# Kernel optimization log

Measured on AMD Instinct MI355X. Metric: run time of the kernel, lower is better.

The kernel has to match this reference:

```python
import jax, jax.numpy as jnp
import numpy as np

N = 50000      # nodes
E = 600000     # edges
C = 32         # in_features (channels)
COUT = 32      # out_features
NB = 8         # n_basis
NS = 10        # n_species
H = 64         # radial MLP hidden
NPATH = 5      # uvu paths for l_max=1: (0,0,0),(0,1,1),(1,0,1),(1,1,0),(1,1,1)
AVG = 12.0     # avg_n_neighbors
RS = 1.6765324703310907  # rescaled SiLU constant


def _rescaled_silu(x):
    return RS * jax.nn.silu(x)


def setup_inputs() -> dict:
    key = jax.random.key(0)
    ks = jax.random.split(key, 16)
    return {
        'node_attrs': jax.random.uniform(ks[0], (N, NS), dtype=jnp.float32),
        'node_feats': jax.random.normal(ks[1], (N, C, 4), dtype=jnp.float32),
        'edge_attrs': jax.random.normal(ks[2], (E, 1, 4), dtype=jnp.float32),
        'edge_feats': jax.random.normal(ks[3], (E, NB), dtype=jnp.float32),
        'W_first': jax.random.normal(ks[4], (2, C, C), dtype=jnp.float32),
        'Wr0': jax.random.normal(ks[5], (H, NB), dtype=jnp.float32),
        'Wr1': jax.random.normal(ks[6], (H, H), dtype=jnp.float32),
        'Wr2': jax.random.normal(ks[7], (H, H), dtype=jnp.float32),
        'Wr3': jax.random.normal(ks[8], (NPATH * C, H), dtype=jnp.float32),
        'W_second0': jax.random.normal(ks[9], (COUT, 2 * C), dtype=jnp.float32),
        'W_second1': jax.random.normal(ks[10], (COUT, 3 * C), dtype=jnp.float32),
        'W_skip': jax.random.normal(ks[11], (2, C, NS, C), dtype=jnp.float32),
        'idx_i': jnp.sort(jax.random.randint(ks[12], (E,), 0, N)),
        'idx_j': jax.random.randint(ks[13], (E,), 0, N),
    }


def reference(node_attrs, node_feats, edge_attrs, edge_feats, W_first, Wr0, Wr1,
              Wr2, Wr3, W_second0, W_second1, W_skip, idx_i, idx_j):
    # ---- skip_tp: uvw tensor product with l=0 node_attrs (species-dependent mixing per l)
    sc0 = jnp.einsum('ncm,nv,cvw->nwm', node_feats[:, :, :1], node_attrs, W_skip[0]) / np.sqrt(C * NS)
    sc1 = jnp.einsum('ncm,nv,cvw->nwm', node_feats[:, :, 1:4], node_attrs, W_skip[1]) / np.sqrt(C * NS)
    sc = jnp.concatenate([sc0, sc1], axis=-1)  # [N, C, 4]

    # ---- linear_first: per-l channel mixing
    x0 = jnp.einsum('ncm,dc->ndm', node_feats[:, :, :1], W_first[0]) / np.sqrt(C)   # [N,C,1]
    x1 = jnp.einsum('ncm,dc->ndm', node_feats[:, :, 1:4], W_first[1]) / np.sqrt(C)  # [N,C,3]

    # ---- radial MLP: Linear+RescaledSiLU chain, last SiLU dropped
    h = _rescaled_silu(edge_feats @ Wr0.T / np.sqrt(NB))
    h = _rescaled_silu(h @ Wr1.T / np.sqrt(H))
    h = _rescaled_silu(h @ Wr2.T / np.sqrt(H))
    w = (h @ Wr3.T / np.sqrt(H)).reshape(E, NPATH, C)  # per-edge, per-path, per-channel weights

    # ---- gather sender features
    xj0 = x0[idx_j][:, :, 0]   # [E, C]
    xj1 = x1[idx_j]            # [E, C, 3]
    y0 = edge_attrs[:, 0, 0]   # [E]      l=0 harmonic
    y1 = edge_attrs[:, 0, 1:4] # [E, 3]   l=1 harmonic

    # ---- uvu weighted tensor product (l_max=1 CG: scalar mult, dot, cross)
    p0 = w[:, 0] * xj0 * y0[:, None]                                   # (0,0,0) -> l=0
    p1 = w[:, 1, :, None] * xj0[:, :, None] * y1[:, None, :]          # (0,1,1) -> l=1
    p2 = w[:, 2, :, None] * xj1 * y0[:, None, None]                   # (1,0,1) -> l=1
    p3 = w[:, 3] * jnp.einsum('ecm,em->ec', xj1, y1)                  # (1,1,0) -> l=0
    p4 = w[:, 4, :, None] * jnp.cross(xj1, y1[:, None, :])            # (1,1,1) -> l=1

    # ---- scatter-add messages to receivers
    seg = lambda m: jax.ops.segment_sum(m, idx_i, num_segments=N)
    msg0 = seg(jnp.stack([p0, p3], axis=1))  # [N, 2, C]
    msg1 = seg(jnp.stack([p1, p2, p4], axis=1))  # [N, 3, C, 3]

    # ---- linear_second: mix (paths x channels) -> out_features per l
    out0 = jnp.einsum('npc,dpc->nd', msg0, W_second0.reshape(COUT, 2, C)) / np.sqrt(2 * C)
    out1 = jnp.einsum('npcm,dpc->ndm', msg1, W_second1.reshape(COUT, 3, C)) / np.sqrt(3 * C)
    message = jnp.concatenate([out0[:, :, None], out1], axis=-1) / AVG  # [N, COUT, 4]
    return message, sc
```

## Files before the change

kernel.cpp:

```cpp
#include <hip/hip_runtime.h>
#include <math.h>

#define N_NODES 50000
#define N_EDGES 600000

constexpr float RS          = 1.6765324703310907f;
constexpr float INV_SQRT8   = 0.35355339059327373f;
constexpr float INV8        = 0.125f;
constexpr float INV_SQRT320 = 0.05590169943749474f;
constexpr float INV_SQRT32  = 0.17677669529663687f;
constexpr float INV_SQRT96  = 0.10206207261596575f;
constexpr float INV_AVG     = 1.0f / 12.0f;

constexpr size_t OFF_X     = 0;
constexpr size_t OFF_ROW   = 25600000;
constexpr size_t OFF_FRAG  = 25800064;
constexpr size_t OFF_FRAG2 = 25841024;
constexpr size_t OFF_W     = 25931136;

typedef __attribute__((ext_vector_type(8))) short bfrag;
typedef __attribute__((ext_vector_type(4))) float ffrag;

__device__ __forceinline__ float rsilu(float z) {
  float t = __builtin_amdgcn_exp2f(z * -1.44269504088896341f);
  return (RS * z) * __builtin_amdgcn_rcpf(1.0f + t);
}
__device__ __forceinline__ unsigned short f2bf(float x) {
  unsigned u = __float_as_uint(x);
  u += 0x7FFFu + ((u >> 16) & 1u);
  return (unsigned short)(u >> 16);
}
__device__ __forceinline__ float bf2f(unsigned short u) {
  return __uint_as_float(((unsigned)u) << 16);
}

__global__ __launch_bounds__(256) void k_rowstart(const int* __restrict__ idx_i,
                                                  int* __restrict__ row,
                                                  int E, int N) {
  int e = blockIdx.x * 256 + threadIdx.x;
  if (e >= E) return;
  int cur  = idx_i[e];
  int prev = (e == 0) ? -1 : idx_i[e - 1];
  for (int n = prev + 1; n <= cur; ++n) row[n] = e;
  if (e == E - 1) {
    for (int n = cur + 1; n <= N; ++n) row[n] = E;
  }
}

__global__ __launch_bounds__(256) void k_prep(const float* __restrict__ Wr0,
                                              const float* __restrict__ Wr1,
                                              const float* __restrict__ Wr2,
                                              const float* __restrict__ Wr3,
                                              unsigned short* __restrict__ frag) {
  int t = blockIdx.x * 256 + threadIdx.x;
  int f    = t >> 9;
  int lane = (t >> 3) & 63;
  int j    = t & 7;
  int n16  = lane & 15, quad = lane >> 4;
  float v;
  if (f < 4) {
    int d = f * 16 + n16, k = quad * 8 + j;
    v = (k < 8) ? Wr0[d * 8 + k] * INV_SQRT8 : 0.f;
  } else if (f < 12) {
    int ff = f - 4, ntile = ff >> 1, ks = ff & 1;
    int d = ntile * 16 + n16, k = ks * 32 + quad * 8 + j;
    v = Wr1[d * 64 + k] * INV8;
  } else if (f < 20) {
    int ff = f - 12, ntile = ff >> 1, ks = ff & 1;
    int d = ntile * 16 + n16, k = ks * 32 + quad * 8 + j;
    v = Wr2[d * 64 + k] * INV8;
  } else {
    int ff = f - 20, ntile = ff >> 1, ks = ff & 1;
    int d = ntile * 16 + n16, k = ks * 32 + quad * 8 + j;
    v = Wr3[d * 64 + k] * INV8;
  }
  frag[t] = f2bf(v);
}

__global__ __launch_bounds__(256) void k_prep2(const float* __restrict__ Wsk,
                                               const float* __restrict__ Wf,
                                               unsigned short* __restrict__ frag2) {
  int t = blockIdx.x * 256 + threadIdx.x;
  int f    = t >> 9;
  int lane = (t >> 3) & 63;
  int j    = t & 7;
  int n16  = lane & 15, quad = lane >> 4;
  int ks = f >> 3, nt = f & 7;
  int k   = ks * 32 + quad * 8 + j;
  int col = nt * 16 + n16;
  float v = 0.f;
  if (k < 320) {
    int vv = k >> 5, c = k & 31;
    if (col < 32)       v = Wsk[(c * 10 + vv) * 32 + col] * INV_SQRT320;
    else if (col < 64)  v = Wsk[((32 + c) * 10 + vv) * 32 + (col - 32)] * INV_SQRT320;
  } else {
    int c = k - 320;
    if (col >= 96)      v = Wf[1024 + (col - 96) * 32 + c] * INV_SQRT32;
    else if (col >= 64) v = Wf[(col - 64) * 32 + c] * INV_SQRT32;
  }
  frag2[t] = f2bf(v);
}

__global__ __launch_bounds__(256) void k_node_mfma(const float* __restrict__ attrs,
                                                   const float* __restrict__ feats,
                                                   const unsigned short* __restrict__ frag2,
                                                   float* __restrict__ out_sc,
                                                   float* __restrict__ x_ws) {
  int tid = threadIdx.x;
  int wave = tid >> 6, lane = tid & 63;
  int quad = lane >> 4, l16 = lane & 15;
  int nb = blockIdx.x * 32 + wave * 8;

  float featsF[2][8];
  float a[2][10];
#pragma unroll
  for (int mt = 0; mt < 2; ++mt) {
    int nodeA = nb + mt * 4 + (l16 >> 2);
    if (nodeA > N_NODES - 1) nodeA = N_NODES - 1;
    int m = l16 & 3;
#pragma unroll
    for (int j = 0; j < 8; ++j)
      featsF[mt][j] = feats[(size_t)nodeA * 128 + (quad * 8 + j) * 4 + m];
#pragma unroll
    for (int v = 0; v < 10; ++v) a[mt][v] = attrs[nodeA * 10 + v];
  }

  ffrag acc[2][8];
#pragma unroll
  for (int mt = 0; mt < 2; ++mt)
#pragma unroll
    for (int nt = 0; nt < 8; ++nt) acc[mt][nt] = (ffrag){0.f, 0.f, 0.f, 0.f};

#pragma unroll
  for (int ks = 0; ks < 11; ++ks) {
    bfrag Ab[2];
#pragma unroll
    for (int mt = 0; mt < 2; ++mt) {
      union { unsigned short s8[8]; bfrag v; } pk;
#pragma unroll
      for (int j = 0; j < 8; ++j) {
        float val = (ks < 10) ? a[mt][ks] * featsF[mt][j] : featsF[mt][j];
        pk.s8[j] = f2bf(val);
      }
      Ab[mt] = pk.v;
    }
#pragma unroll
    for (int nt = 0; nt < 8; ++nt) {
      bfrag B = *(const bfrag*)(frag2 + ((size_t)(ks * 8 + nt) * 64 + lane) * 8);
      acc[0][nt] = __builtin_amdgcn_mfma_f32_16x16x32_bf16(Ab[0], B, acc[0][nt], 0, 0, 0);
      acc[1][nt] = __builtin_amdgcn_mfma_f32_16x16x32_bf16(Ab[1], B, acc[1][nt], 0, 0, 0);
    }
  }

#pragma unroll
  for (int mt = 0; mt < 2; ++mt) {
    int node = nb + mt * 4 + quad;
    if (node < N_NODES) {
      float4 sc0 = {acc[mt][0][0], acc[mt][2][1], acc[mt][2][2], acc[mt][2][3]};
      float4 sc1 = {acc[mt][1][0], acc[mt][3][1], acc[mt][3][2], acc[mt][3][3]};
      float4 x0  = {acc[mt][4][0], acc[mt][6][1], acc[mt][6][2], acc[mt][6][3]};
      float4 x1  = {acc[mt][5][0], acc[mt][7][1], acc[mt][7][2], acc[mt][7][3]};
      ((float4*)out_sc)[(size_t)node * 32 + l16]      = sc0;
      ((float4*)out_sc)[(size_t)node * 32 + 16 + l16] = sc1;
      ((float4*)x_ws)[(size_t)node * 32 + l16]        = x0;
      ((float4*)x_ws)[(size_t)node * 32 + 16 + l16]   = x1;
    }
  }
}

#define MLP_M 128
__global__ __launch_bounds__(256) void k_mlp(const float* __restrict__ ef,
                                             const unsigned short* __restrict__ frag,
                                             unsigned short* __restrict__ w_out,
                                             int E) {
  __shared__ __align__(16) unsigned short H[4][32][168];
  int tid = threadIdx.x;
  int wave = tid >> 6, lane = tid & 63;
  int quad = lane >> 4, l16 = lane & 15;
  int m0 = blockIdx.x * MLP_M + wave * 32;
  unsigned short (*Hw)[168] = H[wave];

  bfrag a1[2];
#pragma unroll
  for (int mt = 0; mt < 2; ++mt) {
    float vals[8] = {0.f, 0.f, 0.f, 0.f, 0.f, 0.f, 0.f, 0.f};
    if (quad == 0) {
      int r = m0 + mt * 16 + l16;
      if (r > E - 1) r = E - 1;
      const float4* p = (const float4*)(ef + (size_t)r * 8);
      float4 u0 = p[0], u1 = p[1];
      vals[0] = u0.x; vals[1] = u0.y; vals[2] = u0.z; vals[3] = u0.w;
      vals[4] = u1.x; vals[5] = u1.y; vals[6] = u1.z; vals[7] = u1.w;
    }
    union { unsigned short s[8]; bfrag v; } pk;
#pragma unroll
    for (int j = 0; j < 8; ++j) pk.s[j] = f2bf(vals[j]);
    a1[mt] = pk.v;
  }
#pragma unroll
  for (int nt = 0; nt < 4; ++nt) {
    const bfrag* bp = (const bfrag*)(frag + ((size_t)(nt) * 64 + lane) * 8);
    bfrag b = *bp;
    ffrag acc0 = {0.f, 0.f, 0.f, 0.f}, acc1 = acc0;
    acc0 = __builtin_amdgcn_mfma_f32_16x16x32_bf16(a1[0], b, acc0, 0, 0, 0);
    acc1 = __builtin_amdgcn_mfma_f32_16x16x32_bf16(a1[1], b, acc1, 0, 0, 0);
#pragma unroll
    for (int r = 0; r < 4; ++r) {
      Hw[0 * 16 + quad * 4 + r][nt * 16 + l16] = f2bf(rsilu(acc0[r]));
      Hw[1 * 16 + quad * 4 + r][nt * 16 + l16] = f2bf(rsilu(acc1[r]));
    }
  }

  bfrag A[2][2];
#pragma unroll 1
  for (int L = 0; L < 2; ++L) {
    int fbase = 4 + L * 8;
#pragma unroll
    for (int mt = 0; mt < 2; ++mt)
#pragma unroll
      for (int ks = 0; ks < 2; ++ks)
        A[mt][ks] = *(const bfrag*)&Hw[mt * 16 + l16][ks * 32 + quad * 8];
#pragma unroll
    for (int nt = 0; nt < 4; ++nt) {
      ffrag acc0 = {0.f, 0.f, 0.f, 0.f}, acc1 = acc0;
#pragma unroll
      for (int ks = 0; ks < 2; ++ks) {
        bfrag b = *(const bfrag*)(frag + ((size_t)(fbase + nt * 2 + ks) * 64 + lane) * 8);
        acc0 = __builtin_amdgcn_mfma_f32_16x16x32_bf16(A[0][ks], b, acc0, 0, 0, 0);
        acc1 = __builtin_amdgcn_mfma_f32_16x16x32_bf16(A[1][ks], b, acc1, 0, 0, 0);
      }
#pragma unroll
      for (int r = 0; r < 4; ++r) {
        Hw[0 * 16 + quad * 4 + r][nt * 16 + l16] = f2bf(rsilu(acc0[r]));
        Hw[1 * 16 + quad * 4 + r][nt * 16 + l16] = f2bf(rsilu(acc1[r]));
      }
    }
  }

#pragma unroll
  for (int mt = 0; mt < 2; ++mt)
#pragma unroll
    for (int ks = 0; ks < 2; ++ks)
      A[mt][ks] = *(const bfrag*)&Hw[mt * 16 + l16][ks * 32 + quad * 8];
#pragma unroll 2
  for (int nt = 0; nt < 10; ++nt) {
    ffrag acc0 = {0.f, 0.f, 0.f, 0.f}, acc1 = acc0;
#pragma unroll
    for (int ks = 0; ks < 2; ++ks) {
      bfrag b = *(const bfrag*)(frag + ((size_t)(20 + nt * 2 + ks) * 64 + lane) * 8);
      acc0 = __builtin_amdgcn_mfma_f32_16x16x32_bf16(A[0][ks], b, acc0, 0, 0, 0);
      acc1 = __builtin_amdgcn_mfma_f32_16x16x32_bf16(A[1][ks], b, acc1, 0, 0, 0);
    }
    int col = nt * 16 + l16;
    int p = col >> 5, cc = col & 31;
    int ncol = (p < 4) ? ((p >> 1) * 64 + 2 * cc + (p & 1)) : (128 + cc);
#pragma unroll
    for (int r = 0; r < 4; ++r) {
      Hw[0 * 16 + quad * 4 + r][ncol] = f2bf(acc0[r]);
      Hw[1 * 16 + quad * 4 + r][ncol] = f2bf(acc1[r]);
    }
  }

  {
    int row = lane / 20, off = lane - row * 20;
    int grow_base = m0;
#pragma unroll 2
    for (int it = 0; it < 10; ++it) {
      int grow = grow_base + row;
      uint4 v = *(const uint4*)&Hw[row][off * 8];
      if (grow < E)
        *(uint4*)(w_out + (size_t)grow * 160 + off * 8) = v;
      off += 4;
      row += 3;
      if (off >= 20) { off -= 20; row += 1; }
    }
  }
}

__global__ __launch_bounds__(256) void k_msg(const unsigned short* __restrict__ w_ws,
                                             const float* __restrict__ x_ws,
                                             const float* __restrict__ ea,
                                             const int* __restrict__ idx_j,
                                             const int* __restrict__ row,
                                             const float* __restrict__ Ws0,
                                             const float* __restrict__ Ws1,
                                             float* __restrict__ out_msg) {
  __shared__ __align__(16) float msg[8][356];

  int tid = threadIdx.x;
  int ln = tid >> 5, c = tid & 31;
  int n = blockIdx.x * 8 + ln;
  int e0 = row[n], e1 = row[n + 1];

  float m00 = 0.f, m01 = 0.f;
  float m10x = 0.f, m10y = 0.f, m10z = 0.f;
  float m11x = 0.f, m11y = 0.f, m11z = 0.f;
  float m12x = 0.f, m12y = 0.f, m12z = 0.f;

  for (int base = e0; base < e1; base += 32) {
    int rem = e1 - base;
    int cnt = rem < 32 ? rem : 32;
    int jidx = base + (c < cnt ? c : cnt - 1);
    int j_c = __builtin_nontemporal_load(idx_j + jidx);

    for (int b = 0; b < cnt; b += 4) {
      int mvalid = cnt - b;
      float4 xj[4], y4[4];
      unsigned d01[4], d23[4];
      unsigned short w4v[4];
#pragma unroll
      for (int t = 0; t < 4; ++t) {
        int tt = (t < mvalid) ? t : 0;
        int e = base + b + tt;
        int j = __shfl(j_c, b + tt, 32);
        xj[t] = ((const float4*)x_ws)[(size_t)j * 32 + c];
        y4[t] = ((const float4*)ea)[e];
        const char* wb = (const char*)w_ws + (size_t)e * 320;
        d01[t] = *(const unsigned*)(wb + 4 * c);
        d23[t] = *(const unsigned*)(wb + 128 + 4 * c);
        w4v[t] = *(const unsigned short*)(wb + 256 + 2 * c);
      }
#pragma unroll
      for (int t = 0; t < 4; ++t) {
        if (t < mvalid) {
          float w0 = __uint_as_float(d01[t] << 16);
          float w1 = __uint_as_float(d01[t] & 0xffff0000u);
          float w2 = __uint_as_float(d23[t] << 16);
          float w3 = __uint_as_float(d23[t] & 0xffff0000u);
          float w4 = bf2f(w4v[t]);
          float4 x4 = xj[t], yy = y4[t];
          m00 += w0 * x4.x * yy.x;
          m01 += w3 * (x4.y * yy.y + x4.z * yy.z + x4.w * yy.w);
          m10x += w1 * x4.x * yy.y;
          m10y += w1 * x4.x * yy.z;
          m10z += w1 * x4.x * yy.w;
          m11x += w2 * x4.y * yy.x;
          m11y += w2 * x4.z * yy.x;
          m11z += w2 * x4.w * yy.x;
          float cx = x4.z * yy.w - x4.w * yy.z;
          float cy = x4.w * yy.y - x4.y * yy.w;
          float cz = x4.y * yy.z - x4.z * yy.y;
          m12x += w4 * cx;
          m12y += w4 * cy;
          m12z += w4 * cz;
        }
      }
    }
  }

  msg[ln][c]      = m00;
  msg[ln][32 + c] = m01;
  msg[ln][64 + 0 * 96 +  0 + c] = m10x;
  msg[ln][64 + 0 * 96 + 32 + c] = m11x;
  msg[ln][64 + 0 * 96 + 64 + c] = m12x;
  msg[ln][64 + 1 * 96 +  0 + c] = m10y;
  msg[ln][64 + 1 * 96 + 32 + c] = m11y;
  msg[ln][64 + 1 * 96 + 64 + c] = m12y;
  msg[ln][64 + 2 * 96 +  0 + c] = m10z;
  msg[ln][64 + 2 * 96 + 32 + c] = m11z;
  msg[ln][64 + 2 * 96 + 64 + c] = m12z;
  __syncthreads();

  int wv = tid >> 6;
  int lane = tid & 63;
  int quad = lane >> 4, l16 = lane & 15;
  int nb = blockIdx.x * 8;

  const float* WS   = (wv == 0) ? Ws0 : Ws1;
  int   K      = (wv == 0) ? 64 : 96;
  int   mbase  = (wv == 0) ? 0 : 64 + (wv - 1) * 96;
  float oscale = (wv == 0) ? (INV8 * INV_AVG) : (INV_SQRT96 * INV_AVG);

  ffrag acc0 = {0.f, 0.f, 0.f, 0.f}, acc1 = acc0;
  const float* arow = &msg[l16 & 7][mbase + quad * 8];
#pragma unroll 1
  for (int ks = 0; ks < K; ks += 32) {
    float4 a0 = *(const float4*)(arow + ks);
    float4 a1 = *(const float4*)(arow + ks + 4);
    union { unsigned short s[8]; bfrag v; } pa;
    pa.s[0] = f2bf(a0.x); pa.s[1] = f2bf(a0.y); pa.s[2] = f2bf(a0.z); pa.s[3] = f2bf(a0.w);
    pa.s[4] = f2bf(a1.x); pa.s[5] = f2bf(a1.y); pa.s[6] = f2bf(a1.z); pa.s[7] = f2bf(a1.w);

    const float* bp0 = WS + (size_t)l16 * K + ks + quad * 8;
    const float* bp1 = bp0 + (size_t)16 * K;
    {
      float4 b0 = *(const float4*)(bp0);
      float4 b1 = *(const float4*)(bp0 + 4);
      union { unsigned short s[8]; bfrag v; } pb;
      pb.s[0] = f2bf(b0.x * oscale); pb.s[1] = f2bf(b0.y * oscale);
      pb.s[2] = f2bf(b0.z * oscale); pb.s[3] = f2bf(b0.w * oscale);
      pb.s[4] = f2bf(b1.x * oscale); pb.s[5] = f2bf(b1.y * oscale);
      pb.s[6] = f2bf(b1.z * oscale); pb.s[7] = f2bf(b1.w * oscale);
      acc0 = __builtin_amdgcn_mfma_f32_16x16x32_bf16(pa.v, pb.v, acc0, 0, 0, 0);
    }
    {
      float4 b0 = *(const float4*)(bp1);
      float4 b1 = *(const float4*)(bp1 + 4);
      union { unsigned short s[8]; bfrag v; } pb;
      pb.s[0] = f2bf(b0.x * oscale); pb.s[1] = f2bf(b0.y * oscale);
      pb.s[2] = f2bf(b0.z * oscale); pb.s[3] = f2bf(b0.w * oscale);
      pb.s[4] = f2bf(b1.x * oscale); pb.s[5] = f2bf(b1.y * oscale);
      pb.s[6] = f2bf(b1.z * oscale); pb.s[7] = f2bf(b1.w * oscale);
      acc1 = __builtin_amdgcn_mfma_f32_16x16x32_bf16(pa.v, pb.v, acc1, 0, 0, 0);
    }
  }

#pragma unroll
  for (int r = 0; r < 4; ++r) {
    int rowv = quad * 4 + r;
    if (rowv < 8) {
      size_t base = (size_t)(nb + rowv) * 128 + (size_t)l16 * 4 + wv;
      out_msg[base]      = acc0[r];
      out_msg[base + 64] = acc1[r];
    }
  }
}

extern "C" void kernel_launch(void* const* d_in, const int* in_sizes, int n_in,
                              void* d_out, int out_size, void* d_ws, size_t ws_size,
                              hipStream_t stream) {
  const float* node_attrs = (const float*)d_in[0];
  const float* node_feats = (const float*)d_in[1];
  const float* edge_attrs = (const float*)d_in[2];
  const float* edge_feats = (const float*)d_in[3];
  const float* W_first    = (const float*)d_in[4];
  const float* Wr0        = (const float*)d_in[5];
  const float* Wr1        = (const float*)d_in[6];
  const float* Wr2        = (const float*)d_in[7];
  const float* Wr3        = (const float*)d_in[8];
  const float* Ws0        = (const float*)d_in[9];
  const float* Ws1        = (const float*)d_in[10];
  const float* Wsk        = (const float*)d_in[11];
  const int*   idx_i      = (const int*)d_in[12];
  const int*   idx_j      = (const int*)d_in[13];
  float* out = (float*)d_out;

  char* ws = (char*)d_ws;
  float*          x_ws   = (float*)(ws + OFF_X);
  int*            rowp   = (int*)(ws + OFF_ROW);
  unsigned short* fragp  = (unsigned short*)(ws + OFF_FRAG);
  unsigned short* frag2p = (unsigned short*)(ws + OFF_FRAG2);
  unsigned short* w_ws   = (unsigned short*)(ws + OFF_W);

  k_rowstart<<<(N_EDGES + 255) / 256, 256, 0, stream>>>(idx_i, rowp, N_EDGES, N_NODES);
  k_prep<<<80, 256, 0, stream>>>(Wr0, Wr1, Wr2, Wr3, fragp);
  k_prep2<<<176, 256, 0, stream>>>(Wsk, W_first, frag2p);
  k_node_mfma<<<(N_NODES + 31) / 32, 256, 0, stream>>>(node_attrs, node_feats,
                                                       frag2p, out + 6400000, x_ws);
  k_mlp<<<(N_EDGES + MLP_M - 1) / MLP_M, 256, 0, stream>>>(edge_feats, fragp,
                                                           w_ws, N_EDGES);
  k_msg<<<N_NODES / 8, 256, 0, stream>>>(w_ws, x_ws, edge_attrs, idx_j, rowp,
                                         Ws0, Ws1, out);
}
```

Before: 333.7 us.

## Assign one full wavefront per node in k_msg, splitting edges across half-waves

The message kernel now gives each node a 64-lane wavefront instead of a 32-lane half-wave. The two halves process alternating groups of 4 edges and combine their partial sums with a cross-half shuffle before writing to shared memory. Block size doubles to 512, and only the first 4 waves run the output MFMA stage. This is meant to shorten the per-node serial edge loop and expose more memory-level parallelism for the gathers, at the cost of more threads per node, idle waves in the epilogue, and extra reduction shuffles.

```diff
diff --git a/kernel.cpp b/kernel.cpp
--- a/kernel.cpp
+++ b/kernel.cpp
@@ -277,7 +277,7 @@
   }
 }
 
-__global__ __launch_bounds__(256) void k_msg(const unsigned short* __restrict__ w_ws,
+__global__ __launch_bounds__(512) void k_msg(const unsigned short* __restrict__ w_ws,
                                              const float* __restrict__ x_ws,
                                              const float* __restrict__ ea,
                                              const int* __restrict__ idx_j,
@@ -288,8 +288,11 @@
   __shared__ __align__(16) float msg[8][356];
 
   int tid = threadIdx.x;
-  int ln = tid >> 5, c = tid & 31;
-  int n = blockIdx.x * 8 + ln;
+  int wv = tid >> 6;
+  int lane = tid & 63;
+  int c = lane & 31;
+  int h = lane >> 5;
+  int n = blockIdx.x * 8 + wv;
   int e0 = row[n], e1 = row[n + 1];
 
   float m00 = 0.f, m01 = 0.f;
@@ -297,22 +300,23 @@
   float m11x = 0.f, m11y = 0.f, m11z = 0.f;
   float m12x = 0.f, m12y = 0.f, m12z = 0.f;
 
-  for (int base = e0; base < e1; base += 32) {
+  for (int base = e0; base < e1; base += 64) {
     int rem = e1 - base;
-    int cnt = rem < 32 ? rem : 32;
-    int jidx = base + (c < cnt ? c : cnt - 1);
+    int cnt = rem < 64 ? rem : 64;
+    int jidx = base + (lane < cnt ? lane : cnt - 1);
     int j_c = __builtin_nontemporal_load(idx_j + jidx);
 
-    for (int b = 0; b < cnt; b += 4) {
-      int mvalid = cnt - b;
+    for (int bb = 0; bb < cnt; bb += 8) {
+      int off0 = bb + h * 4;
       float4 xj[4], y4[4];
       unsigned d01[4], d23[4];
       unsigned short w4v[4];
 #pragma unroll
       for (int t = 0; t < 4; ++t) {
-        int tt = (t < mvalid) ? t : 0;
-        int e = base + b + tt;
-        int j = __shfl(j_c, b + tt, 32);
+        int eo = off0 + t;
+        if (eo > cnt - 1) eo = cnt - 1;
+        int e = base + eo;
+        int j = __shfl(j_c, eo, 64);
         xj[t] = ((const float4*)x_ws)[(size_t)j * 32 + c];
         y4[t] = ((const float4*)ea)[e];
         const char* wb = (const char*)w_ws + (size_t)e * 320;
@@ -322,7 +326,7 @@
       }
 #pragma unroll
       for (int t = 0; t < 4; ++t) {
-        if (t < mvalid) {
+        if (off0 + t < cnt) {
           float w0 = __uint_as_float(d01[t] << 16);
           float w1 = __uint_as_float(d01[t] & 0xffff0000u);
           float w2 = __uint_as_float(d23[t] << 16);
@@ -348,70 +352,84 @@
     }
   }
 
-  msg[ln][c]      = m00;
-  msg[ln][32 + c] = m01;
-  msg[ln][64 + 0 * 96 +  0 + c] = m10x;
-  msg[ln][64 + 0 * 96 + 32 + c] = m11x;
-  msg[ln][64 + 0 * 96 + 64 + c] = m12x;
-  msg[ln][64 + 1 * 96 +  0 + c] = m10y;
-  msg[ln][64 + 1 * 96 + 32 + c] = m11y;
-  msg[ln][64 + 1 * 96 + 64 + c] = m12y;
-  msg[ln][64 + 2 * 96 +  0 + c] = m10z;
-  msg[ln][64 + 2 * 96 + 32 + c] = m11z;
-  msg[ln][64 + 2 * 96 + 64 + c] = m12z;
+  m00  += __shfl_xor(m00, 32, 64);
+  m01  += __shfl_xor(m01, 32, 64);
+  m10x += __shfl_xor(m10x, 32, 64);
+  m10y += __shfl_xor(m10y, 32, 64);
+  m10z += __shfl_xor(m10z, 32, 64);
+  m11x += __shfl_xor(m11x, 32, 64);
+  m11y += __shfl_xor(m11y, 32, 64);
+  m11z += __shfl_xor(m11z, 32, 64);
+  m12x += __shfl_xor(m12x, 32, 64);
+  m12y += __shfl_xor(m12y, 32, 64);
+  m12z += __shfl_xor(m12z, 32, 64);
+
+  if (h == 0) {
+    msg[wv][c]      = m00;
+    msg[wv][32 + c] = m01;
+    msg[wv][64 + 0 * 96 +  0 + c] = m10x;
+    msg[wv][64 + 0 * 96 + 32 + c] = m11x;
+    msg[wv][64 + 0 * 96 + 64 + c] = m12x;
+    msg[wv][64 + 1 * 96 +  0 + c] = m10y;
+    msg[wv][64 + 1 * 96 + 32 + c] = m11y;
+    msg[wv][64 + 1 * 96 + 64 + c] = m12y;
+    msg[wv][64 + 2 * 96 +  0 + c] = m10z;
+    msg[wv][64 + 2 * 96 + 32 + c] = m11z;
+    msg[wv][64 + 2 * 96 + 64 + c] = m12z;
+  }
   __syncthreads();
 
-  int wv = tid >> 6;
-  int lane = tid & 63;
-  int quad = lane >> 4, l16 = lane & 15;
-  int nb = blockIdx.x * 8;
-
-  const float* WS   = (wv == 0) ? Ws0 : Ws1;
-  int   K      = (wv == 0) ? 64 : 96;
-  int   mbase  = (wv == 0) ? 0 : 64 + (wv - 1) * 96;
-  float oscale = (wv == 0) ? (INV8 * INV_AVG) : (INV_SQRT96 * INV_AVG);
-
-  ffrag acc0 = {0.f, 0.f, 0.f, 0.f}, acc1 = acc0;
-  const float* arow = &msg[l16 & 7][mbase + quad * 8];
+  if (wv < 4) {
+    int quad = lane >> 4, l16 = lane & 15;
+    int nb = blockIdx.x * 8;
+
+    const float* WS   = (wv == 0) ? Ws0 : Ws1;
+    int   K      = (wv == 0) ? 64 : 96;
+    int   mbase  = (wv == 0) ? 0 : 64 + (wv - 1) * 96;
+    float oscale = (wv == 0) ? (INV8 * INV_AVG) : (INV_SQRT96 * INV_AVG);
+
+    ffrag acc0 = {0.f, 0.f, 0.f, 0.f}, acc1 = acc0;
+    const float* arow = &msg[l16 & 7][mbase + quad * 8];
 #pragma unroll 1
-  for (int ks = 0; ks < K; ks += 32) {
-    float4 a0 = *(const float4*)(arow + ks);
-    float4 a1 = *(const float4*)(arow + ks + 4);
-    union { unsigned short s[8]; bfrag v; } pa;
-    pa.s[0] = f2bf(a0.x); pa.s[1] = f2bf(a0.y); pa.s[2] = f2bf(a0.z); pa.s[3] = f2bf(a0.w);
-    pa.s[4] = f2bf(a1.x); pa.s[5] = f2bf(a1.y); pa.s[6] = f2bf(a1.z); pa.s[7] = f2bf(a1.w);
-
-    const float* bp0 = WS + (size_t)l16 * K + ks + quad * 8;
-    const float* bp1 = bp0 + (size_t)16 * K;
-    {
-      float4 b0 = *(const float4*)(bp0);
-      float4 b1 = *(const float4*)(bp0 + 4);
-      union { unsigned short s[8]; bfrag v; } pb;
-      pb.s[0] = f2bf(b0.x * oscale); pb.s[1] = f2bf(b0.y * oscale);
-      pb.s[2] = f2bf(b0.z * oscale); pb.s[3] = f2bf(b0.w * oscale);
-      pb.s[4] = f2bf(b1.x * oscale); pb.s[5] = f2bf(b1.y * oscale);
-      pb.s[6] = f2bf(b1.z * oscale); pb.s[7] = f2bf(b1.w * oscale);
-      acc0 = __builtin_amdgcn_mfma_f32_16x16x32_bf16(pa.v, pb.v, acc0, 0, 0, 0);
-    }
-    {
-      float4 b0 = *(const float4*)(bp1);
-      float4 b1 = *(const float4*)(bp1 + 4);
-      union { unsigned short s[8]; bfrag v; } pb;
-      pb.s[0] = f2bf(b0.x * oscale); pb.s[1] = f2bf(b0.y * oscale);
-      pb.s[2] = f2bf(b0.z * oscale); pb.s[3] = f2bf(b0.w * oscale);
-      pb.s[4] = f2bf(b1.x * oscale); pb.s[5] = f2bf(b1.y * oscale);
-      pb.s[6] = f2bf(b1.z * oscale); pb.s[7] = f2bf(b1.w * oscale);
-      acc1 = __builtin_amdgcn_mfma_f32_16x16x32_bf16(pa.v, pb.v, acc1, 0, 0, 0);
-    }
-  }
-
-#pragma unroll
-  for (int r = 0; r < 4; ++r) {
-    int rowv = quad * 4 + r;
-    if (rowv < 8) {
-      size_t base = (size_t)(nb + rowv) * 128 + (size_t)l16 * 4 + wv;
-      out_msg[base]      = acc0[r];
-      out_msg[base + 64] = acc1[r];
+    for (int ks = 0; ks < K; ks += 32) {
+      float4 a0 = *(const float4*)(arow + ks);
+      float4 a1 = *(const float4*)(arow + ks + 4);
+      union { unsigned short s[8]; bfrag v; } pa;
+      pa.s[0] = f2bf(a0.x); pa.s[1] = f2bf(a0.y); pa.s[2] = f2bf(a0.z); pa.s[3] = f2bf(a0.w);
+      pa.s[4] = f2bf(a1.x); pa.s[5] = f2bf(a1.y); pa.s[6] = f2bf(a1.z); pa.s[7] = f2bf(a1.w);
+
+      const float* bp0 = WS + (size_t)l16 * K + ks + quad * 8;
+      const float* bp1 = bp0 + (size_t)16 * K;
+      {
+        float4 b0 = *(const float4*)(bp0);
+        float4 b1 = *(const float4*)(bp0 + 4);
+        union { unsigned short s[8]; bfrag v; } pb;
+        pb.s[0] = f2bf(b0.x * oscale); pb.s[1] = f2bf(b0.y * oscale);
+        pb.s[2] = f2bf(b0.z * oscale); pb.s[3] = f2bf(b0.w * oscale);
+        pb.s[4] = f2bf(b1.x * oscale); pb.s[5] = f2bf(b1.y * oscale);
+        pb.s[6] = f2bf(b1.z * oscale); pb.s[7] = f2bf(b1.w * oscale);
+        acc0 = __builtin_amdgcn_mfma_f32_16x16x32_bf16(pa.v, pb.v, acc0, 0, 0, 0);
+      }
+      {
+        float4 b0 = *(const float4*)(bp1);
+        float4 b1 = *(const float4*)(bp1 + 4);
+        union { unsigned short s[8]; bfrag v; } pb;
+        pb.s[0] = f2bf(b0.x * oscale); pb.s[1] = f2bf(b0.y * oscale);
+        pb.s[2] = f2bf(b0.z * oscale); pb.s[3] = f2bf(b0.w * oscale);
+        pb.s[4] = f2bf(b1.x * oscale); pb.s[5] = f2bf(b1.y * oscale);
+        pb.s[6] = f2bf(b1.z * oscale); pb.s[7] = f2bf(b1.w * oscale);
+        acc1 = __builtin_amdgcn_mfma_f32_16x16x32_bf16(pa.v, pb.v, acc1, 0, 0, 0);
+      }
+    }
+
+#pragma unroll
+    for (int r = 0; r < 4; ++r) {
+      int rowv = quad * 4 + r;
+      if (rowv < 8) {
+        size_t base = (size_t)(nb + rowv) * 128 + (size_t)l16 * 4 + wv;
+        out_msg[base]      = acc0[r];
+        out_msg[base + 64] = acc1[r];
+      }
     }
   }
 }
@@ -449,6 +467,6 @@
                                                        frag2p, out + 6400000, x_ws);
   k_mlp<<<(N_EDGES + MLP_M - 1) / MLP_M, 256, 0, stream>>>(edge_feats, fragp,
                                                            w_ws, N_EDGES);
-  k_msg<<<N_NODES / 8, 256, 0, stream>>>(w_ws, x_ws, edge_attrs, idx_j, rowp,
+  k_msg<<<N_NODES / 8, 512, 0, stream>>>(w_ws, x_ws, edge_attrs, idx_j, rowp,
                                          Ws0, Ws1, out);
 }
```

Measured after the change: 337.2 us. No clear change (+1.0%).

## Fuse radial MLP into message kernel, keeping edge weights in shared memory

Applied to the files above, without the earlier changes.

The radial MLP kernel and the message/scatter kernel are merged. Each 8-node block computes MLP weights for its edge range in 128-edge chunks into LDS, then consumes them directly, so the bf16 per-edge weight buffer no longer round-trips through global memory. In exchange, each chunk adds two block-wide barriers, and per-block MLP work is uneven. LDS use per block also grows, which may lower occupancy.

```diff
diff --git a/kernel.cpp b/kernel.cpp
--- a/kernel.cpp
+++ b/kernel.cpp
@@ -16,7 +16,6 @@
 constexpr size_t OFF_ROW   = 25600000;
 constexpr size_t OFF_FRAG  = 25800064;
 constexpr size_t OFF_FRAG2 = 25841024;
-constexpr size_t OFF_W     = 25931136;
 
 typedef __attribute__((ext_vector_type(8))) short bfrag;
 typedef __attribute__((ext_vector_type(4))) float ffrag;
@@ -168,128 +167,26 @@
   }
 }
 
-#define MLP_M 128
-__global__ __launch_bounds__(256) void k_mlp(const float* __restrict__ ef,
-                                             const unsigned short* __restrict__ frag,
-                                             unsigned short* __restrict__ w_out,
-                                             int E) {
+__global__ __launch_bounds__(256) void k_fused(const float* __restrict__ ef,
+                                               const unsigned short* __restrict__ frag,
+                                               const float* __restrict__ x_ws,
+                                               const float* __restrict__ ea,
+                                               const int* __restrict__ idx_j,
+                                               const int* __restrict__ row,
+                                               const float* __restrict__ Ws0,
+                                               const float* __restrict__ Ws1,
+                                               float* __restrict__ out_msg) {
   __shared__ __align__(16) unsigned short H[4][32][168];
+  __shared__ __align__(16) float msg[8][356];
+
   int tid = threadIdx.x;
   int wave = tid >> 6, lane = tid & 63;
   int quad = lane >> 4, l16 = lane & 15;
-  int m0 = blockIdx.x * MLP_M + wave * 32;
-  unsigned short (*Hw)[168] = H[wave];
-
-  bfrag a1[2];
-#pragma unroll
-  for (int mt = 0; mt < 2; ++mt) {
-    float vals[8] = {0.f, 0.f, 0.f, 0.f, 0.f, 0.f, 0.f, 0.f};
-    if (quad == 0) {
-      int r = m0 + mt * 16 + l16;
-      if (r > E - 1) r = E - 1;
-      const float4* p = (const float4*)(ef + (size_t)r * 8);
-      float4 u0 = p[0], u1 = p[1];
-      vals[0] = u0.x; vals[1] = u0.y; vals[2] = u0.z; vals[3] = u0.w;
-      vals[4] = u1.x; vals[5] = u1.y; vals[6] = u1.z; vals[7] = u1.w;
-    }
-    union { unsigned short s[8]; bfrag v; } pk;
-#pragma unroll
-    for (int j = 0; j < 8; ++j) pk.s[j] = f2bf(vals[j]);
-    a1[mt] = pk.v;
-  }
-#pragma unroll
-  for (int nt = 0; nt < 4; ++nt) {
-    const bfrag* bp = (const bfrag*)(frag + ((size_t)(nt) * 64 + lane) * 8);
-    bfrag b = *bp;
-    ffrag acc0 = {0.f, 0.f, 0.f, 0.f}, acc1 = acc0;
-    acc0 = __builtin_amdgcn_mfma_f32_16x16x32_bf16(a1[0], b, acc0, 0, 0, 0);
-    acc1 = __builtin_amdgcn_mfma_f32_16x16x32_bf16(a1[1], b, acc1, 0, 0, 0);
-#pragma unroll
-    for (int r = 0; r < 4; ++r) {
-      Hw[0 * 16 + quad * 4 + r][nt * 16 + l16] = f2bf(rsilu(acc0[r]));
-      Hw[1 * 16 + quad * 4 + r][nt * 16 + l16] = f2bf(rsilu(acc1[r]));
-    }
-  }
-
-  bfrag A[2][2];
-#pragma unroll 1
-  for (int L = 0; L < 2; ++L) {
-    int fbase = 4 + L * 8;
-#pragma unroll
-    for (int mt = 0; mt < 2; ++mt)
-#pragma unroll
-      for (int ks = 0; ks < 2; ++ks)
-        A[mt][ks] = *(const bfrag*)&Hw[mt * 16 + l16][ks * 32 + quad * 8];
-#pragma unroll
-    for (int nt = 0; nt < 4; ++nt) {
-      ffrag acc0 = {0.f, 0.f, 0.f, 0.f}, acc1 = acc0;
-#pragma unroll
-      for (int ks = 0; ks < 2; ++ks) {
-        bfrag b = *(const bfrag*)(frag + ((size_t)(fbase + nt * 2 + ks) * 64 + lane) * 8);
-        acc0 = __builtin_amdgcn_mfma_f32_16x16x32_bf16(A[0][ks], b, acc0, 0, 0, 0);
-        acc1 = __builtin_amdgcn_mfma_f32_16x16x32_bf16(A[1][ks], b, acc1, 0, 0, 0);
-      }
-#pragma unroll
-      for (int r = 0; r < 4; ++r) {
-        Hw[0 * 16 + quad * 4 + r][nt * 16 + l16] = f2bf(rsilu(acc0[r]));
-        Hw[1 * 16 + quad * 4 + r][nt * 16 + l16] = f2bf(rsilu(acc1[r]));
-      }
-    }
-  }
-
-#pragma unroll
-  for (int mt = 0; mt < 2; ++mt)
-#pragma unroll
-    for (int ks = 0; ks < 2; ++ks)
-      A[mt][ks] = *(const bfrag*)&Hw[mt * 16 + l16][ks * 32 + quad * 8];
-#pragma unroll 2
-  for (int nt = 0; nt < 10; ++nt) {
-    ffrag acc0 = {0.f, 0.f, 0.f, 0.f}, acc1 = acc0;
-#pragma unroll
-    for (int ks = 0; ks < 2; ++ks) {
-      bfrag b = *(const bfrag*)(frag + ((size_t)(20 + nt * 2 + ks) * 64 + lane) * 8);
-      acc0 = __builtin_amdgcn_mfma_f32_16x16x32_bf16(A[0][ks], b, acc0, 0, 0, 0);
-      acc1 = __builtin_amdgcn_mfma_f32_16x16x32_bf16(A[1][ks], b, acc1, 0, 0, 0);
-    }
-    int col = nt * 16 + l16;
-    int p = col >> 5, cc = col & 31;
-    int ncol = (p < 4) ? ((p >> 1) * 64 + 2 * cc + (p & 1)) : (128 + cc);
-#pragma unroll
-    for (int r = 0; r < 4; ++r) {
-      Hw[0 * 16 + quad * 4 + r][ncol] = f2bf(acc0[r]);
-      Hw[1 * 16 + quad * 4 + r][ncol] = f2bf(acc1[r]);
-    }
-  }
-
-  {
-    int row = lane / 20, off = lane - row * 20;
-    int grow_base = m0;
-#pragma unroll 2
-    for (int it = 0; it < 10; ++it) {
-      int grow = grow_base + row;
-      uint4 v = *(const uint4*)&Hw[row][off * 8];
-      if (grow < E)
-        *(uint4*)(w_out + (size_t)grow * 160 + off * 8) = v;
-      off += 4;
-      row += 3;
-      if (off >= 20) { off -= 20; row += 1; }
-    }
-  }
-}
-
-__global__ __launch_bounds__(256) void k_msg(const unsigned short* __restrict__ w_ws,
-                                             const float* __restrict__ x_ws,
-                                             const float* __restrict__ ea,
-                                             const int* __restrict__ idx_j,
-                                             const int* __restrict__ row,
-                                             const float* __restrict__ Ws0,
-                                             const float* __restrict__ Ws1,
-                                             float* __restrict__ out_msg) {
-  __shared__ __align__(16) float msg[8][356];
-
-  int tid = threadIdx.x;
   int ln = tid >> 5, c = tid & 31;
-  int n = blockIdx.x * 8 + ln;
+
+  int nb = blockIdx.x * 8;
+  int e0b = row[nb], e1b = row[nb + 8];
+  int n = nb + ln;
   int e0 = row[n], e1 = row[n + 1];
 
   float m00 = 0.f, m01 = 0.f;
@@ -297,55 +194,149 @@
   float m11x = 0.f, m11y = 0.f, m11z = 0.f;
   float m12x = 0.f, m12y = 0.f, m12z = 0.f;
 
-  for (int base = e0; base < e1; base += 32) {
-    int rem = e1 - base;
-    int cnt = rem < 32 ? rem : 32;
-    int jidx = base + (c < cnt ? c : cnt - 1);
-    int j_c = __builtin_nontemporal_load(idx_j + jidx);
-
-    for (int b = 0; b < cnt; b += 4) {
-      int mvalid = cnt - b;
-      float4 xj[4], y4[4];
-      unsigned d01[4], d23[4];
-      unsigned short w4v[4];
-#pragma unroll
-      for (int t = 0; t < 4; ++t) {
-        int tt = (t < mvalid) ? t : 0;
-        int e = base + b + tt;
-        int j = __shfl(j_c, b + tt, 32);
-        xj[t] = ((const float4*)x_ws)[(size_t)j * 32 + c];
-        y4[t] = ((const float4*)ea)[e];
-        const char* wb = (const char*)w_ws + (size_t)e * 320;
-        d01[t] = *(const unsigned*)(wb + 4 * c);
-        d23[t] = *(const unsigned*)(wb + 128 + 4 * c);
-        w4v[t] = *(const unsigned short*)(wb + 256 + 2 * c);
-      }
-#pragma unroll
-      for (int t = 0; t < 4; ++t) {
-        if (t < mvalid) {
-          float w0 = __uint_as_float(d01[t] << 16);
-          float w1 = __uint_as_float(d01[t] & 0xffff0000u);
-          float w2 = __uint_as_float(d23[t] << 16);
-          float w3 = __uint_as_float(d23[t] & 0xffff0000u);
-          float w4 = bf2f(w4v[t]);
-          float4 x4 = xj[t], yy = y4[t];
-          m00 += w0 * x4.x * yy.x;
-          m01 += w3 * (x4.y * yy.y + x4.z * yy.z + x4.w * yy.w);
-          m10x += w1 * x4.x * yy.y;
-          m10y += w1 * x4.x * yy.z;
-          m10z += w1 * x4.x * yy.w;
-          m11x += w2 * x4.y * yy.x;
-          m11y += w2 * x4.z * yy.x;
-          m11z += w2 * x4.w * yy.x;
-          float cx = x4.z * yy.w - x4.w * yy.z;
-          float cy = x4.w * yy.y - x4.y * yy.w;
-          float cz = x4.y * yy.z - x4.z * yy.y;
-          m12x += w4 * cx;
-          m12y += w4 * cy;
-          m12z += w4 * cz;
-        }
-      }
-    }
+  for (int ck = e0b; ck < e1b; ck += 128) {
+    {
+      unsigned short (*Hw)[168] = H[wave];
+      int m0 = ck + wave * 32;
+
+      bfrag a1[2];
+#pragma unroll
+      for (int mt = 0; mt < 2; ++mt) {
+        float vals[8] = {0.f, 0.f, 0.f, 0.f, 0.f, 0.f, 0.f, 0.f};
+        if (quad == 0) {
+          int r = m0 + mt * 16 + l16;
+          if (r > N_EDGES - 1) r = N_EDGES - 1;
+          const float4* p = (const float4*)(ef + (size_t)r * 8);
+          float4 u0 = p[0], u1 = p[1];
+          vals[0] = u0.x; vals[1] = u0.y; vals[2] = u0.z; vals[3] = u0.w;
+          vals[4] = u1.x; vals[5] = u1.y; vals[6] = u1.z; vals[7] = u1.w;
+        }
+        union { unsigned short s[8]; bfrag v; } pk;
+#pragma unroll
+        for (int j = 0; j < 8; ++j) pk.s[j] = f2bf(vals[j]);
+        a1[mt] = pk.v;
+      }
+#pragma unroll
+      for (int nt = 0; nt < 4; ++nt) {
+        bfrag b = *(const bfrag*)(frag + ((size_t)(nt) * 64 + lane) * 8);
+        ffrag acc0 = {0.f, 0.f, 0.f, 0.f}, acc1 = acc0;
+        acc0 = __builtin_amdgcn_mfma_f32_16x16x32_bf16(a1[0], b, acc0, 0, 0, 0);
+        acc1 = __builtin_amdgcn_mfma_f32_16x16x32_bf16(a1[1], b, acc1, 0, 0, 0);
+#pragma unroll
+        for (int r = 0; r < 4; ++r) {
+          Hw[0 * 16 + quad * 4 + r][nt * 16 + l16] = f2bf(rsilu(acc0[r]));
+          Hw[1 * 16 + quad * 4 + r][nt * 16 + l16] = f2bf(rsilu(acc1[r]));
+        }
+      }
+
+      bfrag A[2][2];
+#pragma unroll 1
+      for (int L = 0; L < 2; ++L) {
+        int fbase = 4 + L * 8;
+#pragma unroll
+        for (int mt = 0; mt < 2; ++mt)
+#pragma unroll
+          for (int ks = 0; ks < 2; ++ks)
+            A[mt][ks] = *(const bfrag*)&Hw[mt * 16 + l16][ks * 32 + quad * 8];
+#pragma unroll
+        for (int nt = 0; nt < 4; ++nt) {
+          ffrag acc0 = {0.f, 0.f, 0.f, 0.f}, acc1 = acc0;
+#pragma unroll
+          for (int ks = 0; ks < 2; ++ks) {
+            bfrag b = *(const bfrag*)(frag + ((size_t)(fbase + nt * 2 + ks) * 64 + lane) * 8);
+            acc0 = __builtin_amdgcn_mfma_f32_16x16x32_bf16(A[0][ks], b, acc0, 0, 0, 0);
+            acc1 = __builtin_amdgcn_mfma_f32_16x16x32_bf16(A[1][ks], b, acc1, 0, 0, 0);
+          }
+#pragma unroll
+          for (int r = 0; r < 4; ++r) {
+            Hw[0 * 16 + quad * 4 + r][nt * 16 + l16] = f2bf(rsilu(acc0[r]));
+            Hw[1 * 16 + quad * 4 + r][nt * 16 + l16] = f2bf(rsilu(acc1[r]));
+          }
+        }
+      }
+
+#pragma unroll
+      for (int mt = 0; mt < 2; ++mt)
+#pragma unroll
+        for (int ks = 0; ks < 2; ++ks)
+          A[mt][ks] = *(const bfrag*)&Hw[mt * 16 + l16][ks * 32 + quad * 8];
+#pragma unroll 2
+      for (int nt = 0; nt < 10; ++nt) {
+        ffrag acc0 = {0.f, 0.f, 0.f, 0.f}, acc1 = acc0;
+#pragma unroll
+        for (int ks = 0; ks < 2; ++ks) {
+          bfrag b = *(const bfrag*)(frag + ((size_t)(20 + nt * 2 + ks) * 64 + lane) * 8);
+          acc0 = __builtin_amdgcn_mfma_f32_16x16x32_bf16(A[0][ks], b, acc0, 0, 0, 0);
+          acc1 = __builtin_amdgcn_mfma_f32_16x16x32_bf16(A[1][ks], b, acc1, 0, 0, 0);
+        }
+        int col = nt * 16 + l16;
+        int p = col >> 5, cc = col & 31;
+        int ncol = (p < 4) ? ((p >> 1) * 64 + 2 * cc + (p & 1)) : (128 + cc);
+#pragma unroll
+        for (int r = 0; r < 4; ++r) {
+          Hw[0 * 16 + quad * 4 + r][ncol] = f2bf(acc0[r]);
+          Hw[1 * 16 + quad * 4 + r][ncol] = f2bf(acc1[r]);
+        }
+      }
+    }
+    __syncthreads();
+
+    {
+      int lo = e0 > ck ? e0 : ck;
+      int hiv = e1 < ck + 128 ? e1 : ck + 128;
+      for (int base = lo; base < hiv; base += 32) {
+        int rem = hiv - base;
+        int cnt = rem < 32 ? rem : 32;
+        int jidx = base + (c < cnt ? c : cnt - 1);
+        int j_c = idx_j[jidx];
+
+        for (int b = 0; b < cnt; b += 4) {
+          int mvalid = cnt - b;
+          float4 xj[4], y4[4];
+          unsigned d01[4], d23[4];
+          unsigned short w4v[4];
+#pragma unroll
+          for (int t = 0; t < 4; ++t) {
+            int tt = (t < mvalid) ? t : 0;
+            int e = base + b + tt;
+            int j = __shfl(j_c, b + tt, 32);
+            xj[t] = ((const float4*)x_ws)[(size_t)j * 32 + c];
+            y4[t] = ((const float4*)ea)[e];
+            int le = e - ck;
+            const unsigned short* wb = &H[le >> 5][le & 31][0];
+            d01[t] = *(const unsigned*)(wb + 2 * c);
+            d23[t] = *(const unsigned*)(wb + 64 + 2 * c);
+            w4v[t] = wb[128 + c];
+          }
+#pragma unroll
+          for (int t = 0; t < 4; ++t) {
+            if (t < mvalid) {
+              float w0 = __uint_as_float(d01[t] << 16);
+              float w1 = __uint_as_float(d01[t] & 0xffff0000u);
+              float w2 = __uint_as_float(d23[t] << 16);
+              float w3 = __uint_as_float(d23[t] & 0xffff0000u);
+              float w4 = bf2f(w4v[t]);
+              float4 x4 = xj[t], yy = y4[t];
+              m00 += w0 * x4.x * yy.x;
+              m01 += w3 * (x4.y * yy.y + x4.z * yy.z + x4.w * yy.w);
+              m10x += w1 * x4.x * yy.y;
+              m10y += w1 * x4.x * yy.z;
+              m10z += w1 * x4.x * yy.w;
+              m11x += w2 * x4.y * yy.x;
+              m11y += w2 * x4.z * yy.x;
+              m11z += w2 * x4.w * yy.x;
+              float cx = x4.z * yy.w - x4.w * yy.z;
+              float cy = x4.w * yy.y - x4.y * yy.w;
+              float cz = x4.y * yy.z - x4.z * yy.y;
+              m12x += w4 * cx;
+              m12y += w4 * cy;
+              m12z += w4 * cz;
+            }
+          }
+        }
+      }
+    }
+    __syncthreads();
   }
 
   msg[ln][c]      = m00;
@@ -361,57 +352,55 @@
   msg[ln][64 + 2 * 96 + 64 + c] = m12z;
   __syncthreads();
 
-  int wv = tid >> 6;
-  int lane = tid & 63;
-  int quad = lane >> 4, l16 = lane & 15;
-  int nb = blockIdx.x * 8;
-
-  const float* WS   = (wv == 0) ? Ws0 : Ws1;
-  int   K      = (wv == 0) ? 64 : 96;
-  int   mbase  = (wv == 0) ? 0 : 64 + (wv - 1) * 96;
-  float oscale = (wv == 0) ? (INV8 * INV_AVG) : (INV_SQRT96 * INV_AVG);
-
-  ffrag acc0 = {0.f, 0.f, 0.f, 0.f}, acc1 = acc0;
-  const float* arow = &msg[l16 & 7][mbase + quad * 8];
+  {
+    int wv = tid >> 6;
+    const float* WS   = (wv == 0) ? Ws0 : Ws1;
+    int   K      = (wv == 0) ? 64 : 96;
+    int   mbase  = (wv == 0) ? 0 : 64 + (wv - 1) * 96;
+    float oscale = (wv == 0) ? (INV8 * INV_AVG) : (INV_SQRT96 * INV_AVG);
+
+    ffrag acc0 = {0.f, 0.f, 0.f, 0.f}, acc1 = acc0;
+    const float* arow = &msg[l16 & 7][mbase + quad * 8];
 #pragma unroll 1
-  for (int ks = 0; ks < K; ks += 32) {
-    float4 a0 = *(const float4*)(arow + ks);
-    float4 a1 = *(const float4*)(arow + ks + 4);
-    union { unsigned short s[8]; bfrag v; } pa;
-    pa.s[0] = f2bf(a0.x); pa.s[1] = f2bf(a0.y); pa.s[2] = f2bf(a0.z); pa.s[3] = f2bf(a0.w);
-    pa.s[4] = f2bf(a1.x); pa.s[5] = f2bf(a1.y); pa.s[6] = f2bf(a1.z); pa.s[7] = f2bf(a1.w);
-
-    const float* bp0 = WS + (size_t)l16 * K + ks + quad * 8;
-    const float* bp1 = bp0 + (size_t)16 * K;
-    {
-      float4 b0 = *(const float4*)(bp0);
-      float4 b1 = *(const float4*)(bp0 + 4);
-      union { unsigned short s[8]; bfrag v; } pb;
-      pb.s[0] = f2bf(b0.x * oscale); pb.s[1] = f2bf(b0.y * oscale);
-      pb.s[2] = f2bf(b0.z * oscale); pb.s[3] = f2bf(b0.w * oscale);
-      pb.s[4] = f2bf(b1.x * oscale); pb.s[5] = f2bf(b1.y * oscale);
-      pb.s[6] = f2bf(b1.z * oscale); pb.s[7] = f2bf(b1.w * oscale);
-      acc0 = __builtin_amdgcn_mfma_f32_16x16x32_bf16(pa.v, pb.v, acc0, 0, 0, 0);
-    }
-    {
-      float4 b0 = *(const float4*)(bp1);
-      float4 b1 = *(const float4*)(bp1 + 4);
-      union { unsigned short s[8]; bfrag v; } pb;
-      pb.s[0] = f2bf(b0.x * oscale); pb.s[1] = f2bf(b0.y * oscale);
-      pb.s[2] = f2bf(b0.z * oscale); pb.s[3] = f2bf(b0.w * oscale);
-      pb.s[4] = f2bf(b1.x * oscale); pb.s[5] = f2bf(b1.y * oscale);
-      pb.s[6] = f2bf(b1.z * oscale); pb.s[7] = f2bf(b1.w * oscale);
-      acc1 = __builtin_amdgcn_mfma_f32_16x16x32_bf16(pa.v, pb.v, acc1, 0, 0, 0);
-    }
-  }
-
-#pragma unroll
-  for (int r = 0; r < 4; ++r) {
-    int rowv = quad * 4 + r;
-    if (rowv < 8) {
-      size_t base = (size_t)(nb + rowv) * 128 + (size_t)l16 * 4 + wv;
-      out_msg[base]      = acc0[r];
-      out_msg[base + 64] = acc1[r];
+    for (int ks = 0; ks < K; ks += 32) {
+      float4 a0 = *(const float4*)(arow + ks);
+      float4 a1 = *(const float4*)(arow + ks + 4);
+      union { unsigned short s[8]; bfrag v; } pa;
+      pa.s[0] = f2bf(a0.x); pa.s[1] = f2bf(a0.y); pa.s[2] = f2bf(a0.z); pa.s[3] = f2bf(a0.w);
+      pa.s[4] = f2bf(a1.x); pa.s[5] = f2bf(a1.y); pa.s[6] = f2bf(a1.z); pa.s[7] = f2bf(a1.w);
+
+      const float* bp0 = WS + (size_t)l16 * K + ks + quad * 8;
+      const float* bp1 = bp0 + (size_t)16 * K;
+      {
+        float4 b0 = *(const float4*)(bp0);
+        float4 b1 = *(const float4*)(bp0 + 4);
+        union { unsigned short s[8]; bfrag v; } pb;
+        pb.s[0] = f2bf(b0.x * oscale); pb.s[1] = f2bf(b0.y * oscale);
+        pb.s[2] = f2bf(b0.z * oscale); pb.s[3] = f2bf(b0.w * oscale);
+        pb.s[4] = f2bf(b1.x * oscale); pb.s[5] = f2bf(b1.y * oscale);
+        pb.s[6] = f2bf(b1.z * oscale); pb.s[7] = f2bf(b1.w * oscale);
+        acc0 = __builtin_amdgcn_mfma_f32_16x16x32_bf16(pa.v, pb.v, acc0, 0, 0, 0);
+      }
+      {
+        float4 b0 = *(const float4*)(bp1);
+        float4 b1 = *(const float4*)(bp1 + 4);
+        union { unsigned short s[8]; bfrag v; } pb;
+        pb.s[0] = f2bf(b0.x * oscale); pb.s[1] = f2bf(b0.y * oscale);
+        pb.s[2] = f2bf(b0.z * oscale); pb.s[3] = f2bf(b0.w * oscale);
+        pb.s[4] = f2bf(b1.x * oscale); pb.s[5] = f2bf(b1.y * oscale);
+        pb.s[6] = f2bf(b1.z * oscale); pb.s[7] = f2bf(b1.w * oscale);
+        acc1 = __builtin_amdgcn_mfma_f32_16x16x32_bf16(pa.v, pb.v, acc1, 0, 0, 0);
+      }
+    }
+
+#pragma unroll
+    for (int r = 0; r < 4; ++r) {
+      int rowv = quad * 4 + r;
+      if (rowv < 8) {
+        size_t base = (size_t)(nb + rowv) * 128 + (size_t)l16 * 4 + (size_t)(tid >> 6);
+        out_msg[base]      = acc0[r];
+        out_msg[base + 64] = acc1[r];
+      }
     }
   }
 }
@@ -440,15 +429,12 @@
   int*            rowp   = (int*)(ws + OFF_ROW);
   unsigned short* fragp  = (unsigned short*)(ws + OFF_FRAG);
   unsigned short* frag2p = (unsigned short*)(ws + OFF_FRAG2);
-  unsigned short* w_ws   = (unsigned short*)(ws + OFF_W);
 
   k_rowstart<<<(N_EDGES + 255) / 256, 256, 0, stream>>>(idx_i, rowp, N_EDGES, N_NODES);
   k_prep<<<80, 256, 0, stream>>>(Wr0, Wr1, Wr2, Wr3, fragp);
   k_prep2<<<176, 256, 0, stream>>>(Wsk, W_first, frag2p);
   k_node_mfma<<<(N_NODES + 31) / 32, 256, 0, stream>>>(node_attrs, node_feats,
                                                        frag2p, out + 6400000, x_ws);
-  k_mlp<<<(N_EDGES + MLP_M - 1) / MLP_M, 256, 0, stream>>>(edge_feats, fragp,
-                                                           w_ws, N_EDGES);
-  k_msg<<<N_NODES / 8, 256, 0, stream>>>(w_ws, x_ws, edge_attrs, idx_j, rowp,
-                                         Ws0, Ws1, out);
-}
+  k_fused<<<N_NODES / 8, 256, 0, stream>>>(edge_feats, fragp, x_ws, edge_attrs,
+                                           idx_j, rowp, Ws0, Ws1, out);
+}
```

After: 359.0 us. +7.6%, slower.
